# Performance work log

Measured on AMD Instinct MI355X. Metric: run time of the kernel, lower is better.

## Reference

```python
import jax, jax.numpy as jnp
import numpy as np

T = 35            # cfg.VOXEL_POINT_COUNT
D, H, W = 10, 400, 352  # cfg.INPUT_DEPTH/HEIGHT/WIDTH
EPS = 1e-5


def _vfe(x, mask, w, b, gamma, beta):
    # x: [K, T, Cin]; mask: [K, T, 1]
    h = jax.nn.relu(jnp.einsum('ktc,cu->ktu', x, w) + b)        # [K, T, U]
    mean = jnp.mean(h, axis=(0, 1))
    var = jnp.var(h, axis=(0, 1))
    h = (h - mean) * jax.lax.rsqrt(var + EPS) * gamma + beta    # batch-stat BN
    agg = jnp.max(h, axis=1, keepdims=True)                     # [K, 1, U]
    cat = jnp.concatenate([h, jnp.broadcast_to(agg, h.shape)], axis=-1)  # [K, T, 2U]
    return cat * mask


def setup_inputs() -> dict:
    key = jax.random.key(0)
    ks = jax.random.split(key, 12)
    K = 40000
    feature = jax.random.normal(ks[0], (K, T, 7), dtype=jnp.float32)
    # zero out ~half the points so the nonzero mask is meaningful
    keep = jax.random.bernoulli(ks[1], 0.5, (K, T, 1)).astype(jnp.float32)
    feature = feature * keep
    bidx = jax.random.randint(ks[2], (K, 1), 0, 2)
    didx = jax.random.randint(ks[3], (K, 1), 0, D)
    hidx = jax.random.randint(ks[4], (K, 1), 0, H)
    widx = jax.random.randint(ks[5], (K, 1), 0, W)
    coordinate = jnp.concatenate([bidx, didx, hidx, widx], axis=1).astype(jnp.int32)
    s = 0.1
    return {
        'feature': feature,
        'w1': jax.random.normal(ks[6], (7, 16), dtype=jnp.float32) * s,
        'b1': jnp.zeros((16,), dtype=jnp.float32),
        'gamma1': jnp.ones((16,), dtype=jnp.float32),
        'beta1': jnp.zeros((16,), dtype=jnp.float32),
        'w2': jax.random.normal(ks[7], (32, 32), dtype=jnp.float32) * s,
        'b2': jnp.zeros((32,), dtype=jnp.float32),
        'gamma2': jnp.ones((32,), dtype=jnp.float32),
        'beta2': jnp.zeros((32,), dtype=jnp.float32),
        'coordinate': coordinate,
        'batch_size': 2,
    }


def reference(feature, w1, b1, gamma1, beta1, w2, b2, gamma2, beta2, coordinate, batch_size):
    # mask: voxel point is valid if any channel nonzero (max over channels != 0)
    mask = (jnp.max(feature, axis=2, keepdims=True) != 0).astype(feature.dtype)  # [K, T, 1]
    x = _vfe(feature, mask, w1, b1, gamma1, beta1)   # [K, T, 32]
    x = _vfe(x, mask, w2, b2, gamma2, beta2)         # [K, T, 64]
    voxelwise = jnp.max(x, axis=1)                   # [K, 64]
    out = jnp.zeros((batch_size, D, H, W, 64), dtype=voxelwise.dtype)
    out = out.at[coordinate[:, 0], coordinate[:, 1], coordinate[:, 2], coordinate[:, 3]].add(voxelwise)
    return out
```

## Files before the change

### kernel.cpp

```cpp
#include <hip/hip_runtime.h>
#include <math.h>

#define TT 35
#define DD 10
#define HD 400
#define WD 352
#define CIN 7
#define U1 16
#define U2 32
#define EPSV 1e-5f

#define WS_SUM1 256
#define WS_SSQ1 768
#define WS_SUM2 1280
#define WS_SSQ2 1792
#define NC1 32
#define NC2 16
#define WS_ZERO_FLOATS 2304
#define WS_H2_OFF_FLOATS 4096
#define MASK_STRIDE 36

typedef __bf16 bf16x8 __attribute__((ext_vector_type(8)));
typedef float f32x4 __attribute__((ext_vector_type(4)));

__device__ inline float bf2f(unsigned short b) {
  unsigned u = ((unsigned)b) << 16;
  return __builtin_bit_cast(float, u);
}
__device__ inline unsigned short f2bf(float x) {
  unsigned u = __builtin_bit_cast(unsigned, x);
  unsigned r = (u + 0x7fff + ((u >> 16) & 1)) >> 16;
  return (unsigned short)r;
}

__global__ __launch_bounds__(256) void k_stats1(
    const float* __restrict__ feat, const float* __restrict__ w1,
    const float* __restrict__ b1, float* __restrict__ ws, int P) {
  __shared__ float s_w1[CIN * U1];
  __shared__ float s_b1[U1];
  __shared__ float s_red[4][2 * U1];

  int tid = threadIdx.x;
  if (tid < CIN * U1) s_w1[tid] = w1[tid];
  if (tid < U1) s_b1[tid] = b1[tid];
  __syncthreads();

  float sum[U1], ssq[U1];
#pragma unroll
  for (int u = 0; u < U1; ++u) { sum[u] = 0.f; ssq[u] = 0.f; }

  int stride = gridDim.x * blockDim.x;
  for (int p = blockIdx.x * blockDim.x + tid; p < P; p += stride) {
    const float* f = feat + (size_t)p * CIN;
    float x[CIN];
#pragma unroll
    for (int c = 0; c < CIN; ++c) x[c] = f[c];
#pragma unroll
    for (int u = 0; u < U1; ++u) {
      float acc = s_b1[u];
#pragma unroll
      for (int c = 0; c < CIN; ++c) acc += x[c] * s_w1[c * U1 + u];
      float h = fmaxf(acc, 0.f);
      sum[u] += h;
      ssq[u] += h * h;
    }
  }

  int lane = tid & 63, wv = tid >> 6;
#pragma unroll
  for (int u = 0; u < U1; ++u) {
    float s = sum[u], q = ssq[u];
    for (int off = 32; off; off >>= 1) {
      s += __shfl_down(s, off);
      q += __shfl_down(q, off);
    }
    if (lane == 0) { s_red[wv][u] = s; s_red[wv][U1 + u] = q; }
  }
  __syncthreads();
  if (tid < 2 * U1) {
    float tot = s_red[0][tid] + s_red[1][tid] + s_red[2][tid] + s_red[3][tid];
    int copy = blockIdx.x & (NC1 - 1);
    int u = tid & (U1 - 1);
    int base = (tid < U1) ? WS_SUM1 : WS_SSQ1;
    atomicAdd(&ws[base + copy * U1 + u], tot);
  }
}

__global__ __launch_bounds__(256) void k_vfe2(
    const float* __restrict__ feat, const float* __restrict__ w1,
    const float* __restrict__ b1, const float* __restrict__ g1,
    const float* __restrict__ be1, const float* __restrict__ w2,
    const float* __restrict__ b2, float* __restrict__ ws,
    unsigned short* __restrict__ h2g, float* __restrict__ maskg,
    float4* __restrict__ out4, long n4, int K, float invN) {
  __shared__ unsigned short s_w2b[32 * 40];
  __shared__ unsigned short s_catb[4][48][32];
  __shared__ float s_red[4][64];

  int tid = threadIdx.x;
  int lane = tid & 63, wv = tid >> 6;
  int g = lane >> 4, u = lane & 15;
  int v = blockIdx.x * 4 + wv;
  bool active = (v < K);

  for (int i = tid; i < 32 * 32; i += 256) {
    int n = i >> 5, cp = i & 31;
    int c = (cp & 1) ? (16 + (cp >> 1)) : (cp >> 1);
    s_w2b[n * 40 + cp] = f2bf(w2[c * 32 + n]);
  }
  {
    unsigned* z = (unsigned*)s_catb;
    for (int i = tid; i < 4 * 13 * 16; i += 256) {
      int w = i / 208, rem = i % 208;
      int row = 35 + (rem >> 4), k = rem & 15;
      z[(w * 48 + row) * 16 + k] = 0u;
    }
  }

  float s1 = 0.f, q1 = 0.f;
#pragma unroll
  for (int c = 0; c < NC1; ++c) {
    s1 += ws[WS_SUM1 + c * U1 + u];
    q1 += ws[WS_SSQ1 + c * U1 + u];
  }
  float mean1 = s1 * invN;
  float var1 = q1 * invN - mean1 * mean1;
  float A1 = g1[u] / sqrtf(var1 + EPSV);
  float B1 = be1[u] - mean1 * A1;

  float w1r[CIN];
#pragma unroll
  for (int c = 0; c < CIN; ++c) w1r[c] = w1[c * U1 + u];
  float b1u = b1[u];

  float h1n[9], mkv[9];
  float aggl = -INFINITY;
  const float* fv = feat + (size_t)v * (TT * CIN);
#pragma unroll
  for (int j = 0; j < 9; ++j) {
    int t = g + 4 * j;
    h1n[j] = -INFINITY;
    mkv[j] = 0.f;
    if (active && t < TT) {
      const float* fr = fv + t * CIN;
      float x0 = fr[0], x1 = fr[1], x2 = fr[2], x3 = fr[3];
      float x4 = fr[4], x5 = fr[5], x6 = fr[6];
      float m = fmaxf(fmaxf(fmaxf(x0, x1), fmaxf(x2, x3)),
                      fmaxf(fmaxf(x4, x5), x6));
      float mk = (m != 0.f) ? 1.f : 0.f;
      float acc = b1u + x0 * w1r[0] + x1 * w1r[1] + x2 * w1r[2] +
                  x3 * w1r[3] + x4 * w1r[4] + x5 * w1r[5] + x6 * w1r[6];
      float h = fmaxf(acc, 0.f);
      h1n[j] = A1 * h + B1;
      mkv[j] = mk;
      if (u == 0) maskg[(size_t)v * MASK_STRIDE + t] = mk;
      aggl = fmaxf(aggl, h1n[j]);
    }
  }
  aggl = fmaxf(aggl, __shfl_xor(aggl, 16));
  aggl = fmaxf(aggl, __shfl_xor(aggl, 32));

#pragma unroll
  for (int j = 0; j < 9; ++j) {
    int t = g + 4 * j;
    if (active && t < TT) {
      unsigned pk = (unsigned)f2bf(h1n[j] * mkv[j]) |
                    ((unsigned)f2bf(aggl * mkv[j]) << 16);
      *(unsigned*)&s_catb[wv][t][2 * u] = pk;
    }
  }
  __syncthreads();

  f32x4 acc[2][3];
#pragma unroll
  for (int nt = 0; nt < 2; ++nt)
#pragma unroll
    for (int mt = 0; mt < 3; ++mt) acc[nt][mt] = (f32x4)(0.f);

  bf16x8 bfr[2];
#pragma unroll
  for (int nt = 0; nt < 2; ++nt) {
    uint4 raw = *(const uint4*)&s_w2b[(nt * 16 + u) * 40 + g * 8];
    bfr[nt] = __builtin_bit_cast(bf16x8, raw);
  }
#pragma unroll
  for (int mt = 0; mt < 3; ++mt) {
    uint4 raw = *(const uint4*)&s_catb[wv][mt * 16 + u][g * 8];
    bf16x8 afr = __builtin_bit_cast(bf16x8, raw);
#pragma unroll
    for (int nt = 0; nt < 2; ++nt)
      acc[nt][mt] =
          __builtin_amdgcn_mfma_f32_16x16x32_bf16(afr, bfr[nt], acc[nt][mt], 0, 0, 0);
  }

  float b2c[2] = {b2[u], b2[16 + u]};
  float sum[2] = {0.f, 0.f}, ssq[2] = {0.f, 0.f};
#pragma unroll
  for (int nt = 0; nt < 2; ++nt) {
#pragma unroll
    for (int mt = 0; mt < 3; ++mt) {
      unsigned pk[2];
      float hv[4];
#pragma unroll
      for (int r = 0; r < 4; ++r) {
        int row = mt * 16 + g * 4 + r;
        float h = fmaxf(acc[nt][mt][r] + b2c[nt], 0.f);
        hv[r] = h;
        if (row < TT) {
          sum[nt] += h;
          ssq[nt] += h * h;
        }
      }
      pk[0] = (unsigned)f2bf(hv[0]) | ((unsigned)f2bf(hv[1]) << 16);
      pk[1] = (unsigned)f2bf(hv[2]) | ((unsigned)f2bf(hv[3]) << 16);
      if (active) {
        uint2 st = make_uint2(pk[0], pk[1]);
        *(uint2*)&h2g[((size_t)v * 6 + nt * 3 + mt) * 256 + lane * 4] = st;
      }
    }
  }

#pragma unroll
  for (int nt = 0; nt < 2; ++nt) {
    sum[nt] += __shfl_xor(sum[nt], 16);
    sum[nt] += __shfl_xor(sum[nt], 32);
    ssq[nt] += __shfl_xor(ssq[nt], 16);
    ssq[nt] += __shfl_xor(ssq[nt], 32);
  }
  float contrib = 0.f;
  if (active) {
    contrib = (g == 0) ? sum[0] : (g == 1) ? sum[1] : (g == 2) ? ssq[0] : ssq[1];
  }
  s_red[wv][(g & 1) * 16 + u + (g >> 1) * 32] = contrib;
  __syncthreads();
  if (tid < 64) {
    float tot = s_red[0][tid] + s_red[1][tid] + s_red[2][tid] + s_red[3][tid];
    int copy = blockIdx.x & (NC2 - 1);
    int ch = tid & 31;
    int base = (tid < 32) ? WS_SUM2 : WS_SSQ2;
    atomicAdd(&ws[base + copy * U2 + ch], tot);
  }

  long gtid = (long)blockIdx.x * 256 + tid;
  long gstride = (long)gridDim.x * 256;
  float4 zz = make_float4(0.f, 0.f, 0.f, 0.f);
  for (long i = gtid; i < n4; i += gstride) out4[i] = zz;
}

__global__ __launch_bounds__(256) void k_final(
    const unsigned short* __restrict__ h2g, const float* __restrict__ maskg,
    const float* __restrict__ ws, const float* __restrict__ g2,
    const float* __restrict__ be2, const int* __restrict__ coord,
    float* __restrict__ out, int K, float invN) {
  int tid = threadIdx.x;
  int lane = tid & 63, wv = tid >> 6;
  int g = lane >> 4, u = lane & 15;
  int v = blockIdx.x * 4 + wv;
  if (v >= K) return;

  float A2[2], B2[2];
#pragma unroll
  for (int h = 0; h < 2; ++h) {
    int ch = h * 16 + u;
    float s = 0.f, q = 0.f;
#pragma unroll
    for (int c = 0; c < NC2; ++c) {
      s += ws[WS_SUM2 + c * U2 + ch];
      q += ws[WS_SSQ2 + c * U2 + ch];
    }
    float mean = s * invN;
    float var = q * invN - mean * mean;
    float A = g2[ch] / sqrtf(var + EPSV);
    A2[h] = A;
    B2[h] = be2[ch] - mean * A;
  }

  float vox[2] = {-INFINITY, -INFINITY};
  float agg[2] = {-INFINITY, -INFINITY};
  float cnt = 0.f;
#pragma unroll
  for (int mt = 0; mt < 3; ++mt) {
    const float4 mk4 = *(const float4*)&maskg[(size_t)v * MASK_STRIDE + mt * 16 + g * 4];
    float mk[4] = {mk4.x, mk4.y, mk4.z, mk4.w};
#pragma unroll
    for (int nt = 0; nt < 2; ++nt) {
      uint2 raw = *(const uint2*)&h2g[((size_t)v * 6 + nt * 3 + mt) * 256 + lane * 4];
      unsigned short e[4] = {(unsigned short)(raw.x & 0xffff),
                             (unsigned short)(raw.x >> 16),
                             (unsigned short)(raw.y & 0xffff),
                             (unsigned short)(raw.y >> 16)};
#pragma unroll
      for (int r = 0; r < 4; ++r) {
        int row = mt * 16 + g * 4 + r;
        if (row < TT) {
          float hn = A2[nt] * bf2f(e[r]) + B2[nt];
          agg[nt] = fmaxf(agg[nt], hn);
          vox[nt] = fmaxf(vox[nt], hn * mk[r]);
          if (nt == 0) cnt += mk[r];
        }
      }
    }
  }
#pragma unroll
  for (int nt = 0; nt < 2; ++nt) {
    vox[nt] = fmaxf(vox[nt], __shfl_xor(vox[nt], 16));
    vox[nt] = fmaxf(vox[nt], __shfl_xor(vox[nt], 32));
    agg[nt] = fmaxf(agg[nt], __shfl_xor(agg[nt], 16));
    agg[nt] = fmaxf(agg[nt], __shfl_xor(agg[nt], 32));
  }
  cnt += __shfl_xor(cnt, 16);
  cnt += __shfl_xor(cnt, 32);

  float val;
  if (lane < 32) {
    val = (lane < 16) ? vox[0] : vox[1];
  } else {
    float a = (lane < 48) ? agg[0] : agg[1];
    val = (cnt > 0.5f) ? ((cnt < TT - 0.5f) ? fmaxf(a, 0.f) : a) : 0.f;
  }
  const int4 cd = *(const int4*)&coord[4 * v];
  long base = ((((long)cd.x * DD + cd.y) * HD + cd.z) * WD + cd.w) * 64;
  atomicAdd(&out[base + lane], val);
}

extern "C" void kernel_launch(void* const* d_in, const int* in_sizes, int n_in,
                              void* d_out, int out_size, void* d_ws,
                              size_t ws_size, hipStream_t stream) {
  const float* feat = (const float*)d_in[0];
  const float* w1 = (const float*)d_in[1];
  const float* b1 = (const float*)d_in[2];
  const float* g1 = (const float*)d_in[3];
  const float* be1 = (const float*)d_in[4];
  const float* w2 = (const float*)d_in[5];
  const float* b2 = (const float*)d_in[6];
  const float* g2 = (const float*)d_in[7];
  const float* be2 = (const float*)d_in[8];
  const int* coord = (const int*)d_in[9];
  float* out = (float*)d_out;
  float* ws = (float*)d_ws;

  int K = in_sizes[0] / (TT * CIN);
  int P = K * TT;
  float invN = 1.0f / (float)P;
  long n4 = (long)out_size / 4;

  unsigned short* h2g = (unsigned short*)(ws + WS_H2_OFF_FLOATS);
  float* maskg = (float*)(h2g + (size_t)K * 6 * 256);

  (void)hipMemsetAsync(d_ws, 0, WS_ZERO_FLOATS * sizeof(float), stream);

  k_stats1<<<512, 256, 0, stream>>>(feat, w1, b1, ws, P);

  int vb = (K + 3) / 4;
  k_vfe2<<<vb, 256, 0, stream>>>(feat, w1, b1, g1, be1, w2, b2, ws, h2g, maskg,
                                 (float4*)out, n4, K, invN);
  k_final<<<vb, 256, 0, stream>>>(h2g, maskg, ws, g2, be2, coord, out, K, invN);
}
```

Measured before the change: 911.3 us.

## Replace stored layer-2 activations with per-voxel max/min summaries exploiting affine BN

Instead of writing the full bf16 layer-2 activation tile per voxel and re-reading it in the final kernel, the VFE2 kernel now records per-channel masked and unmasked max/min plus a valid-point count. The final kernel applies the batch-norm affine to max or min depending on the sign of the scale, which reproduces the max after normalization. This removes most of the intermediate global memory traffic and shrinks the final kernel to a small per-channel computation with two atomics per thread. It adds extra shuffle reductions and a shared-memory mask lookup in the VFE2 epilogue.

```diff
diff --git a/kernel.cpp b/kernel.cpp
--- a/kernel.cpp
+++ b/kernel.cpp
@@ -17,16 +17,11 @@
 #define NC1 32
 #define NC2 16
 #define WS_ZERO_FLOATS 2304
-#define WS_H2_OFF_FLOATS 4096
-#define MASK_STRIDE 36
+#define WS_SUM_OFF 4096
 
 typedef __bf16 bf16x8 __attribute__((ext_vector_type(8)));
 typedef float f32x4 __attribute__((ext_vector_type(4)));
 
-__device__ inline float bf2f(unsigned short b) {
-  unsigned u = ((unsigned)b) << 16;
-  return __builtin_bit_cast(float, u);
-}
 __device__ inline unsigned short f2bf(float x) {
   unsigned u = __builtin_bit_cast(unsigned, x);
   unsigned r = (u + 0x7fff + ((u >> 16) & 1)) >> 16;
@@ -91,10 +86,11 @@
     const float* __restrict__ b1, const float* __restrict__ g1,
     const float* __restrict__ be1, const float* __restrict__ w2,
     const float* __restrict__ b2, float* __restrict__ ws,
-    unsigned short* __restrict__ h2g, float* __restrict__ maskg,
+    float* __restrict__ sumg, float* __restrict__ cntg,
     float4* __restrict__ out4, long n4, int K, float invN) {
   __shared__ unsigned short s_w2b[32 * 40];
   __shared__ unsigned short s_catb[4][48][32];
+  __shared__ float s_mk[4][40];
   __shared__ float s_red[4][64];
 
   int tid = threadIdx.x;
@@ -135,6 +131,7 @@
 
   float h1n[9], mkv[9];
   float aggl = -INFINITY;
+  float cntl = 0.f;
   const float* fv = feat + (size_t)v * (TT * CIN);
 #pragma unroll
   for (int j = 0; j < 9; ++j) {
@@ -153,12 +150,16 @@
       float h = fmaxf(acc, 0.f);
       h1n[j] = A1 * h + B1;
       mkv[j] = mk;
-      if (u == 0) maskg[(size_t)v * MASK_STRIDE + t] = mk;
+      cntl += mk;
+      if (u == 0) s_mk[wv][t] = mk;
       aggl = fmaxf(aggl, h1n[j]);
     }
   }
   aggl = fmaxf(aggl, __shfl_xor(aggl, 16));
   aggl = fmaxf(aggl, __shfl_xor(aggl, 32));
+  cntl += __shfl_xor(cntl, 16);
+  cntl += __shfl_xor(cntl, 32);
+  if (active && lane == 0) cntg[v] = cntl;
 
 #pragma unroll
   for (int j = 0; j < 9; ++j) {
@@ -195,27 +196,27 @@
 
   float b2c[2] = {b2[u], b2[16 + u]};
   float sum[2] = {0.f, 0.f}, ssq[2] = {0.f, 0.f};
+  float maxm[2] = {-INFINITY, -INFINITY}, minm[2] = {INFINITY, INFINITY};
+  float maxa[2] = {-INFINITY, -INFINITY}, mina[2] = {INFINITY, INFINITY};
 #pragma unroll
   for (int nt = 0; nt < 2; ++nt) {
 #pragma unroll
     for (int mt = 0; mt < 3; ++mt) {
-      unsigned pk[2];
-      float hv[4];
 #pragma unroll
       for (int r = 0; r < 4; ++r) {
         int row = mt * 16 + g * 4 + r;
-        float h = fmaxf(acc[nt][mt][r] + b2c[nt], 0.f);
-        hv[r] = h;
         if (row < TT) {
+          float h = fmaxf(acc[nt][mt][r] + b2c[nt], 0.f);
           sum[nt] += h;
           ssq[nt] += h * h;
+          maxa[nt] = fmaxf(maxa[nt], h);
+          mina[nt] = fminf(mina[nt], h);
+          float mk = s_mk[wv][row];
+          if (mk != 0.f) {
+            maxm[nt] = fmaxf(maxm[nt], h);
+            minm[nt] = fminf(minm[nt], h);
+          }
         }
-      }
-      pk[0] = (unsigned)f2bf(hv[0]) | ((unsigned)f2bf(hv[1]) << 16);
-      pk[1] = (unsigned)f2bf(hv[2]) | ((unsigned)f2bf(hv[3]) << 16);
-      if (active) {
-        uint2 st = make_uint2(pk[0], pk[1]);
-        *(uint2*)&h2g[((size_t)v * 6 + nt * 3 + mt) * 256 + lane * 4] = st;
       }
     }
   }
@@ -226,7 +227,23 @@
     sum[nt] += __shfl_xor(sum[nt], 32);
     ssq[nt] += __shfl_xor(ssq[nt], 16);
     ssq[nt] += __shfl_xor(ssq[nt], 32);
-  }
+    maxa[nt] = fmaxf(maxa[nt], __shfl_xor(maxa[nt], 16));
+    maxa[nt] = fmaxf(maxa[nt], __shfl_xor(maxa[nt], 32));
+    mina[nt] = fminf(mina[nt], __shfl_xor(mina[nt], 16));
+    mina[nt] = fminf(mina[nt], __shfl_xor(mina[nt], 32));
+    maxm[nt] = fmaxf(maxm[nt], __shfl_xor(maxm[nt], 16));
+    maxm[nt] = fmaxf(maxm[nt], __shfl_xor(maxm[nt], 32));
+    minm[nt] = fminf(minm[nt], __shfl_xor(minm[nt], 16));
+    minm[nt] = fminf(minm[nt], __shfl_xor(minm[nt], 32));
+  }
+  if (active && g == 0) {
+#pragma unroll
+    for (int nt = 0; nt < 2; ++nt) {
+      float4 sm = make_float4(maxm[nt], minm[nt], maxa[nt], mina[nt]);
+      *(float4*)&sumg[(size_t)v * 128 + (nt * 16 + u) * 4] = sm;
+    }
+  }
+
   float contrib = 0.f;
   if (active) {
     contrib = (g == 0) ? sum[0] : (g == 1) ? sum[1] : (g == 2) ? ssq[0] : ssq[1];
@@ -248,79 +265,38 @@
 }
 
 __global__ __launch_bounds__(256) void k_final(
-    const unsigned short* __restrict__ h2g, const float* __restrict__ maskg,
+    const float* __restrict__ sumg, const float* __restrict__ cntg,
     const float* __restrict__ ws, const float* __restrict__ g2,
     const float* __restrict__ be2, const int* __restrict__ coord,
     float* __restrict__ out, int K, float invN) {
   int tid = threadIdx.x;
-  int lane = tid & 63, wv = tid >> 6;
-  int g = lane >> 4, u = lane & 15;
-  int v = blockIdx.x * 4 + wv;
+  int v = blockIdx.x * 8 + (tid >> 5);
+  int ch = tid & 31;
   if (v >= K) return;
 
-  float A2[2], B2[2];
-#pragma unroll
-  for (int h = 0; h < 2; ++h) {
-    int ch = h * 16 + u;
-    float s = 0.f, q = 0.f;
-#pragma unroll
-    for (int c = 0; c < NC2; ++c) {
-      s += ws[WS_SUM2 + c * U2 + ch];
-      q += ws[WS_SSQ2 + c * U2 + ch];
-    }
-    float mean = s * invN;
-    float var = q * invN - mean * mean;
-    float A = g2[ch] / sqrtf(var + EPSV);
-    A2[h] = A;
-    B2[h] = be2[ch] - mean * A;
-  }
-
-  float vox[2] = {-INFINITY, -INFINITY};
-  float agg[2] = {-INFINITY, -INFINITY};
-  float cnt = 0.f;
-#pragma unroll
-  for (int mt = 0; mt < 3; ++mt) {
-    const float4 mk4 = *(const float4*)&maskg[(size_t)v * MASK_STRIDE + mt * 16 + g * 4];
-    float mk[4] = {mk4.x, mk4.y, mk4.z, mk4.w};
-#pragma unroll
-    for (int nt = 0; nt < 2; ++nt) {
-      uint2 raw = *(const uint2*)&h2g[((size_t)v * 6 + nt * 3 + mt) * 256 + lane * 4];
-      unsigned short e[4] = {(unsigned short)(raw.x & 0xffff),
-                             (unsigned short)(raw.x >> 16),
-                             (unsigned short)(raw.y & 0xffff),
-                             (unsigned short)(raw.y >> 16)};
-#pragma unroll
-      for (int r = 0; r < 4; ++r) {
-        int row = mt * 16 + g * 4 + r;
-        if (row < TT) {
-          float hn = A2[nt] * bf2f(e[r]) + B2[nt];
-          agg[nt] = fmaxf(agg[nt], hn);
-          vox[nt] = fmaxf(vox[nt], hn * mk[r]);
-          if (nt == 0) cnt += mk[r];
-        }
-      }
-    }
-  }
-#pragma unroll
-  for (int nt = 0; nt < 2; ++nt) {
-    vox[nt] = fmaxf(vox[nt], __shfl_xor(vox[nt], 16));
-    vox[nt] = fmaxf(vox[nt], __shfl_xor(vox[nt], 32));
-    agg[nt] = fmaxf(agg[nt], __shfl_xor(agg[nt], 16));
-    agg[nt] = fmaxf(agg[nt], __shfl_xor(agg[nt], 32));
-  }
-  cnt += __shfl_xor(cnt, 16);
-  cnt += __shfl_xor(cnt, 32);
-
-  float val;
-  if (lane < 32) {
-    val = (lane < 16) ? vox[0] : vox[1];
-  } else {
-    float a = (lane < 48) ? agg[0] : agg[1];
-    val = (cnt > 0.5f) ? ((cnt < TT - 0.5f) ? fmaxf(a, 0.f) : a) : 0.f;
-  }
+  float s = 0.f, q = 0.f;
+#pragma unroll
+  for (int c = 0; c < NC2; ++c) {
+    s += ws[WS_SUM2 + c * U2 + ch];
+    q += ws[WS_SSQ2 + c * U2 + ch];
+  }
+  float mean = s * invN;
+  float var = q * invN - mean * mean;
+  float A2 = g2[ch] / sqrtf(var + EPSV);
+  float B2 = be2[ch] - mean * A2;
+
+  float4 sm = *(const float4*)&sumg[(size_t)v * 128 + ch * 4];
+  float cnt = cntg[v];
+
+  float hm = (A2 >= 0.f) ? (A2 * sm.x + B2) : (A2 * sm.y + B2);
+  float ag = (A2 >= 0.f) ? (A2 * sm.z + B2) : (A2 * sm.w + B2);
+  float voxr = (cnt < 0.5f) ? 0.f : ((cnt > TT - 0.5f) ? hm : fmaxf(hm, 0.f));
+  float voxa = (cnt < 0.5f) ? 0.f : ((cnt > TT - 0.5f) ? ag : fmaxf(ag, 0.f));
+
   const int4 cd = *(const int4*)&coord[4 * v];
   long base = ((((long)cd.x * DD + cd.y) * HD + cd.z) * WD + cd.w) * 64;
-  atomicAdd(&out[base + lane], val);
+  atomicAdd(&out[base + ch], voxr);
+  atomicAdd(&out[base + 32 + ch], voxa);
 }
 
 extern "C" void kernel_launch(void* const* d_in, const int* in_sizes, int n_in,
@@ -344,15 +320,16 @@
   float invN = 1.0f / (float)P;
   long n4 = (long)out_size / 4;
 
-  unsigned short* h2g = (unsigned short*)(ws + WS_H2_OFF_FLOATS);
-  float* maskg = (float*)(h2g + (size_t)K * 6 * 256);
+  float* sumg = ws + WS_SUM_OFF;
+  float* cntg = sumg + (size_t)K * 128;
 
   (void)hipMemsetAsync(d_ws, 0, WS_ZERO_FLOATS * sizeof(float), stream);
 
   k_stats1<<<512, 256, 0, stream>>>(feat, w1, b1, ws, P);
 
   int vb = (K + 3) / 4;
-  k_vfe2<<<vb, 256, 0, stream>>>(feat, w1, b1, g1, be1, w2, b2, ws, h2g, maskg,
+  k_vfe2<<<vb, 256, 0, stream>>>(feat, w1, b1, g1, be1, w2, b2, ws, sumg, cntg,
                                  (float4*)out, n4, K, invN);
-  k_final<<<vb, 256, 0, stream>>>(h2g, maskg, ws, g2, be2, coord, out, K, invN);
-}
+  k_final<<<(K + 7) / 8, 256, 0, stream>>>(sumg, cntg, ws, g2, be2, coord, out,
+                                           K, invN);
+}
```

Result: faster. 849.9 us (-6.7%).
